# Kernel tuning notes

Hardware: AMD Instinct MI355X
Metric: run time of the kernel (lower is better)

The kernel has to match this reference:

```python
import jax, jax.numpy as jnp
import numpy as np
from jax import lax

ALPHA = 0.85
C1 = 0.01 ** 2
C2 = 0.03 ** 2


def _avg_pool3(x):
    # F.avg_pool2d(x, 3, 1, 1) with count_include_pad=True: zero-pad, divide by 9.
    s = lax.reduce_window(x, jnp.array(0.0, x.dtype), lax.add,
                          (1, 1, 3, 3), (1, 1, 1, 1),
                          [(0, 0), (0, 0), (1, 1), (1, 1)])
    return s / jnp.array(9.0, x.dtype)


def _ssim(x, y):
    mu_x = _avg_pool3(x)
    mu_y = _avg_pool3(y)
    sigma_x = jnp.clip(_avg_pool3(x * x) - mu_x * mu_x, 0.0, None)
    sigma_y = jnp.clip(_avg_pool3(y * y) - mu_y * mu_y, 0.0, None)
    sigma_xy = _avg_pool3(x * y) - mu_x * mu_y
    ssim_n = (2.0 * mu_x * mu_y + C1) * (2.0 * sigma_xy + C2)
    ssim_d = (mu_x * mu_x + mu_y * mu_y + C1) * (sigma_x + sigma_y + C2)
    return jnp.clip((1.0 - ssim_n / ssim_d) / 2.0, 0.0, 1.0)


def _warp_right(right_img, disp):
    # grid_sample(bilinear, border, align_corners=True) where y maps identically
    # to its own row -> a 1D horizontal bilinear gather at x_sample = x - disp.
    B, C, H, W = right_img.shape
    x_base = jnp.arange(W, dtype=disp.dtype).reshape(1, 1, 1, W)
    x_sample = x_base - disp                      # [B,1,H,W]
    xs = jnp.clip(x_sample, 0.0, W - 1.0)         # border padding
    x0 = jnp.floor(xs)
    w = xs - x0                                   # frac weight
    i0 = x0.astype(jnp.int32)
    i1 = jnp.minimum(i0 + 1, W - 1)
    i0b = jnp.broadcast_to(i0, (B, C, H, W))
    i1b = jnp.broadcast_to(i1, (B, C, H, W))
    g0 = jnp.take_along_axis(right_img, i0b, axis=3)
    g1 = jnp.take_along_axis(right_img, i1b, axis=3)
    warped = (1.0 - w) * g0 + w * g1              # w broadcasts over C
    valid = ((x_sample > 0) & (x_sample < W - 1)).astype(disp.dtype)
    return warped, valid


def setup_inputs() -> dict:
    key = jax.random.key(0)
    k1, k2, k3 = jax.random.split(key, 3)
    B, H, W = 8, 720, 1280
    disp = jax.random.normal(k1, (B, 1, H, W), dtype=jnp.float32)
    left_img = jax.random.uniform(k2, (B, 3, H, W), dtype=jnp.float32)
    right_img = jax.random.uniform(k3, (B, 3, H, W), dtype=jnp.float32)
    return {"disp": disp, "left_img": left_img, "right_img": right_img}


def reference(disp, left_img, right_img):
    right_warped, valid = _warp_right(right_img, disp)
    l1_err = jnp.mean(jnp.abs(left_img - right_warped), axis=1, keepdims=True)
    ssim_err = jnp.mean(_ssim(left_img, right_warped), axis=1, keepdims=True)
    photo_err = ALPHA * ssim_err + (1.0 - ALPHA) * l1_err
    n_valid = jnp.maximum(jnp.sum(valid), 1.0)
    return jnp.sum(photo_err * valid) / n_valid
```

## Files before the change

kernel.cpp:

```cpp
#include <hip/hip_runtime.h>


#define P_ALPHA 0.85f
#define P_C1 1e-4f
#define P_C2 9e-4f

constexpr int COLS  = 62;
constexpr int RPW   = 15;
constexpr int WAVES = 4;

__global__ __launch_bounds__(256, 6)
void photo_loss_kernel(const float* __restrict__ disp,
                       const float* __restrict__ left,
                       const float* __restrict__ right,
                       float* __restrict__ acc,
                       int H, int W)
{
    __shared__ float redpv[WAVES];
    __shared__ float redv[WAVES];

    const int tid  = threadIdx.x;
    const int lane = tid & 63;
    const int w    = tid >> 6;
    const int b    = blockIdx.z;
    const int col  = blockIdx.x * COLS + lane - 1;
    const int rowStart = (blockIdx.y * WAVES + w) * RPW;

    const int planeHW = H * W;
    const float* __restrict__ dispb = disp  + b * planeHW;
    const float* __restrict__ L0 = left  + (b * 3 + 0) * planeHW;
    const float* __restrict__ L1 = left  + (b * 3 + 1) * planeHW;
    const float* __restrict__ L2 = left  + (b * 3 + 2) * planeHW;
    const float* __restrict__ R0 = right + (b * 3 + 0) * planeHW;
    const float* __restrict__ R1 = right + (b * 3 + 1) * planeHW;
    const float* __restrict__ R2 = right + (b * 3 + 2) * planeHW;

    const float wm1f = (float)(W - 1);
    const int   colC = min(max(col, 0), W - 1);
    const float colv = (col >= 0 && col < W) ? 1.f : 0.f;
    const float ocm  = (lane >= 1 && lane <= COLS && col < W) ? 1.f : 0.f;

    float Ax0=0.f,Ay0=0.f,Axx0=0.f,Ayy0=0.f,Axy0=0.f;
    float Ax1=0.f,Ay1=0.f,Axx1=0.f,Ayy1=0.f,Axy1=0.f;
    float Ax2=0.f,Ay2=0.f,Axx2=0.f,Ayy2=0.f,Axy2=0.f;
    float Bx0=0.f,By0=0.f,Bxx0=0.f,Byy0=0.f,Bxy0=0.f;
    float Bx1=0.f,By1=0.f,Bxx1=0.f,Byy1=0.f,Bxy1=0.f;
    float Bx2=0.f,By2=0.f,Bxx2=0.f,Byy2=0.f,Bxy2=0.f;
    float l1P=0.f, vP=0.f;

    float sum_pv = 0.f, sum_v = 0.f;

    float gN0,gN1,gN2,gN3,gN4,gN5, frN, vmN, xN0,xN1,xN2;
    float dN;
    int   offN;

    {
        const int   rc0  = max(rowStart - 1, 0);
        const int   off0 = rc0 * W + colC;
        const float d0   = dispb[off0];
        xN0 = L0[off0]; xN1 = L1[off0]; xN2 = L2[off0];
        offN = rowStart * W + colC;
        dN   = dispb[offN];
        const float xs  = (float)col - d0;
        const float xcl = fminf(fmaxf(xs, 0.f), wm1f);
        const float xf  = floorf(xcl);
        frN = xcl - xf;
        const int i0 = (int)xf;
        const int i1 = min(i0 + 1, W - 1);
        const int ro = rc0 * W;
        gN0 = R0[ro + i0]; gN1 = R0[ro + i1];
        gN2 = R1[ro + i0]; gN3 = R1[ro + i1];
        gN4 = R2[ro + i0]; gN5 = R2[ro + i1];
        vmN = (xs > 0.f && xs < wm1f) ? 1.f : 0.f;
    }

    #pragma unroll 2
    for (int j = 0; j < RPW + 2; ++j) {
        const int r = rowStart - 1 + j;

        const float g0=gN0,g1=gN1,g2=gN2,g3=gN3,g4=gN4,g5=gN5;
        const float fr=frN, vm=vmN, xc0=xN0, xc1=xN1, xc2=xN2;

        if (j <= RPW) {
            const float xs  = (float)col - dN;
            const float xcl = fminf(fmaxf(xs, 0.f), wm1f);
            const float xf  = floorf(xcl);
            frN = xcl - xf;
            const int i0 = (int)xf;
            const int i1 = min(i0 + 1, W - 1);
            const int ro = offN - colC;
            gN0 = R0[ro + i0]; gN1 = R0[ro + i1];
            gN2 = R1[ro + i0]; gN3 = R1[ro + i1];
            gN4 = R2[ro + i0]; gN5 = R2[ro + i1];
            vmN = (xs > 0.f && xs < wm1f) ? 1.f : 0.f;
            xN0 = L0[offN]; xN1 = L1[offN]; xN2 = L2[offN];
            const int rc2 = min(r + 2, H - 1);
            offN = rc2 * W + colC;
            dN   = dispb[offN];
        }

        const float rv  = (r >= 0 && r < H) ? 1.f : 0.f;
        const float m   = rv * colv;
        const float omf = 1.f - fr;
        const float y0 = (omf * g0 + fr * g1) * m;
        const float y1 = (omf * g2 + fr * g3) * m;
        const float y2 = (omf * g4 + fr * g5) * m;
        const float x0 = xc0 * m;
        const float x1 = xc1 * m;
        const float x2 = xc2 * m;

        float Cx0,Cy0,Cxx0,Cyy0,Cxy0;
        float Cx1,Cy1,Cxx1,Cyy1,Cxy1;
        float Cx2,Cy2,Cxx2,Cyy2,Cxy2;
        {
            const float xl = __shfl_up(x0,1,64), xr = __shfl_down(x0,1,64);
            const float yl = __shfl_up(y0,1,64), yr = __shfl_down(y0,1,64);
            Cx0  = xl + x0 + xr;
            Cy0  = yl + y0 + yr;
            Cxx0 = xl*xl + x0*x0 + xr*xr;
            Cyy0 = yl*yl + y0*y0 + yr*yr;
            Cxy0 = xl*yl + x0*y0 + xr*yr;
        }
        {
            const float xl = __shfl_up(x1,1,64), xr = __shfl_down(x1,1,64);
            const float yl = __shfl_up(y1,1,64), yr = __shfl_down(y1,1,64);
            Cx1  = xl + x1 + xr;
            Cy1  = yl + y1 + yr;
            Cxx1 = xl*xl + x1*x1 + xr*xr;
            Cyy1 = yl*yl + y1*y1 + yr*yr;
            Cxy1 = xl*yl + x1*y1 + xr*yr;
        }
        {
            const float xl = __shfl_up(x2,1,64), xr = __shfl_down(x2,1,64);
            const float yl = __shfl_up(y2,1,64), yr = __shfl_down(y2,1,64);
            Cx2  = xl + x2 + xr;
            Cy2  = yl + y2 + yr;
            Cxx2 = xl*xl + x2*x2 + xr*xr;
            Cyy2 = yl*yl + y2*y2 + yr*yr;
            Cxy2 = xl*yl + x2*y2 + xr*yr;
        }
        const float l1C = fabsf(x0 - y0) + fabsf(x1 - y1) + fabsf(x2 - y2);
        const float vC  = vm;

        if (j >= 2) {
            const float inv9 = 1.f / 9.f;
            float ssim_sum = 0.f;
            #define SSIM_CH(SX,SY,SXX,SYY,SXY)                                   \
            {                                                                    \
                const float mu_x = (A##SX + B##SX + C##SX) * inv9;               \
                const float mu_y = (A##SY + B##SY + C##SY) * inv9;               \
                const float exx  = (A##SXX + B##SXX + C##SXX) * inv9;            \
                const float eyy  = (A##SYY + B##SYY + C##SYY) * inv9;            \
                const float exy  = (A##SXY + B##SXY + C##SXY) * inv9;            \
                const float sig_x  = fmaxf(exx - mu_x * mu_x, 0.f);              \
                const float sig_y  = fmaxf(eyy - mu_y * mu_y, 0.f);              \
                const float sig_xy = exy - mu_x * mu_y;                          \
                const float n  = (2.f*mu_x*mu_y + P_C1) * (2.f*sig_xy + P_C2);   \
                const float dd = (mu_x*mu_x + mu_y*mu_y + P_C1)                  \
                               * (sig_x + sig_y + P_C2);                         \
                float s = (1.f - n * __builtin_amdgcn_rcpf(dd)) * 0.5f;          \
                s = fminf(fmaxf(s, 0.f), 1.f);                                   \
                ssim_sum += s;                                                   \
            }
            SSIM_CH(x0,y0,xx0,yy0,xy0)
            SSIM_CH(x1,y1,xx1,yy1,xy1)
            SSIM_CH(x2,y2,xx2,yy2,xy2)
            #undef SSIM_CH
            const float photo = P_ALPHA * (ssim_sum * (1.f / 3.f))
                              + (1.f - P_ALPHA) * (l1P * (1.f / 3.f));
            sum_pv += photo * vP * ocm;
            sum_v  += vP * ocm;
        }

        Ax0=Bx0; Ay0=By0; Axx0=Bxx0; Ayy0=Byy0; Axy0=Bxy0;
        Ax1=Bx1; Ay1=By1; Axx1=Bxx1; Ayy1=Byy1; Axy1=Bxy1;
        Ax2=Bx2; Ay2=By2; Axx2=Bxx2; Ayy2=Byy2; Axy2=Bxy2;
        Bx0=Cx0; By0=Cy0; Bxx0=Cxx0; Byy0=Cyy0; Bxy0=Cxy0;
        Bx1=Cx1; By1=Cy1; Bxx1=Cxx1; Byy1=Cyy1; Bxy1=Cxy1;
        Bx2=Cx2; By2=Cy2; Bxx2=Cxx2; Byy2=Cyy2; Bxy2=Cxy2;
        l1P = l1C; vP = vC;
    }

    #pragma unroll
    for (int off = 32; off > 0; off >>= 1) {
        sum_pv += __shfl_down(sum_pv, off, 64);
        sum_v  += __shfl_down(sum_v,  off, 64);
    }
    if (lane == 0) { redpv[w] = sum_pv; redv[w] = sum_v; }
    __syncthreads();
    if (tid == 0) {
        atomicAdd(&acc[0], redpv[0] + redpv[1] + redpv[2] + redpv[3]);
        atomicAdd(&acc[1], redv[0]  + redv[1]  + redv[2]  + redv[3]);
    }
}

__global__ void photo_loss_finalize(const float* __restrict__ acc,
                                    float* __restrict__ out)
{
    out[0] = acc[0] / fmaxf(acc[1], 1.f);
}

extern "C" void kernel_launch(void* const* d_in, const int* in_sizes, int n_in,
                              void* d_out, int out_size, void* d_ws, size_t ws_size,
                              hipStream_t stream)
{
    const float* disp  = (const float*)d_in[0];
    const float* left  = (const float*)d_in[1];
    const float* right = (const float*)d_in[2];
    float* out = (float*)d_out;
    float* acc = (float*)d_ws;

    const int B = 8, H = 720, W = 1280;

    hipMemsetAsync(acc, 0, 2 * sizeof(float), stream);

    dim3 grid((W + COLS - 1) / COLS, H / (WAVES * RPW), B);
    dim3 block(256);
    photo_loss_kernel<<<grid, block, 0, stream>>>(disp, left, right, acc, H, W);
    photo_loss_finalize<<<1, 1, 0, stream>>>(acc, out);
}
```

Baseline: 260.8 us.

## Stage right-image row window in LDS for warp gathers with global fallback

Each wave now loads a padded 80-column window of the three right-image channels per row into double-buffered shared memory using coalesced loads, prefetching one row ahead. The bilinear gathers read from LDS, and lanes whose sample index falls outside the window fall back to direct global loads. This replaces scattered global gathers with coalesced loads plus LDS reads. In exchange it adds LDS traffic, extra registers and a divergent fallback path, and lowers the launch-bounds occupancy hint from 6 to 4.

```diff
diff --git a/kernel.cpp b/kernel.cpp
--- a/kernel.cpp
+++ b/kernel.cpp
@@ -8,14 +8,17 @@
 constexpr int COLS  = 62;
 constexpr int RPW   = 15;
 constexpr int WAVES = 4;
-
-__global__ __launch_bounds__(256, 6)
+constexpr int PADW  = 80;
+constexpr int NST   = 3 * PADW;
+
+__global__ __launch_bounds__(256, 4)
 void photo_loss_kernel(const float* __restrict__ disp,
                        const float* __restrict__ left,
                        const float* __restrict__ right,
                        float* __restrict__ acc,
                        int H, int W)
 {
+    __shared__ float stage[WAVES][2][NST];
     __shared__ float redpv[WAVES];
     __shared__ float redv[WAVES];
 
@@ -23,8 +26,10 @@
     const int lane = tid & 63;
     const int w    = tid >> 6;
     const int b    = blockIdx.z;
-    const int col  = blockIdx.x * COLS + lane - 1;
+    const int s0   = blockIdx.x * COLS;
+    const int col  = s0 + lane - 1;
     const int rowStart = (blockIdx.y * WAVES + w) * RPW;
+    const int W_LO = s0 - 9;
 
     const int planeHW = H * W;
     const float* __restrict__ dispb = disp  + b * planeHW;
@@ -36,9 +41,27 @@
     const float* __restrict__ R2 = right + (b * 3 + 2) * planeHW;
 
     const float wm1f = (float)(W - 1);
+    const float colf = (float)col;
     const int   colC = min(max(col, 0), W - 1);
     const float colv = (col >= 0 && col < W) ? 1.f : 0.f;
     const float ocm  = (lane >= 1 && lane <= COLS && col < W) ? 1.f : 0.f;
+
+    int  sOff[4];
+    int  sLds[4];
+    bool sAct[4];
+    #pragma unroll
+    for (int p = 0; p < 4; ++p) {
+        const int idx  = p * 64 + lane;
+        sAct[p] = (idx < NST);
+        const int idxc = min(idx, NST - 1);
+        const int ch   = idxc / PADW;
+        const int k    = idxc - ch * PADW;
+        const int srcCol = min(max(W_LO + k, 0), W - 1);
+        sOff[p] = (b * 3 + ch) * planeHW + srcCol;
+        sLds[p] = ch * PADW + k;
+    }
+    float* const buf0 = &stage[w][0][0];
+    float* const buf1 = &stage[w][1][0];
 
     float Ax0=0.f,Ay0=0.f,Axx0=0.f,Ayy0=0.f,Axy0=0.f;
     float Ax1=0.f,Ay1=0.f,Axx1=0.f,Ayy1=0.f,Axy1=0.f;
@@ -50,61 +73,72 @@
 
     float sum_pv = 0.f, sum_v = 0.f;
 
-    float gN0,gN1,gN2,gN3,gN4,gN5, frN, vmN, xN0,xN1,xN2;
-    float dN;
-    int   offN;
-
+    float sv0, sv1, sv2, sv3;
+    const int rc0 = max(rowStart - 1, 0);
     {
-        const int   rc0  = max(rowStart - 1, 0);
-        const int   off0 = rc0 * W + colC;
-        const float d0   = dispb[off0];
-        xN0 = L0[off0]; xN1 = L1[off0]; xN2 = L2[off0];
-        offN = rowStart * W + colC;
-        dN   = dispb[offN];
-        const float xs  = (float)col - d0;
-        const float xcl = fminf(fmaxf(xs, 0.f), wm1f);
-        const float xf  = floorf(xcl);
-        frN = xcl - xf;
-        const int i0 = (int)xf;
-        const int i1 = min(i0 + 1, W - 1);
         const int ro = rc0 * W;
-        gN0 = R0[ro + i0]; gN1 = R0[ro + i1];
-        gN2 = R1[ro + i0]; gN3 = R1[ro + i1];
-        gN4 = R2[ro + i0]; gN5 = R2[ro + i1];
-        vmN = (xs > 0.f && xs < wm1f) ? 1.f : 0.f;
+        sv0 = right[sOff[0] + ro];
+        sv1 = right[sOff[1] + ro];
+        sv2 = right[sOff[2] + ro];
+        sv3 = sAct[3] ? right[sOff[3] + ro] : 0.f;
+        buf0[sLds[0]] = sv0; buf0[sLds[1]] = sv1; buf0[sLds[2]] = sv2;
+        if (sAct[3]) buf0[sLds[3]] = sv3;
+    }
+    {
+        const int ro = rowStart * W;
+        sv0 = right[sOff[0] + ro];
+        sv1 = right[sOff[1] + ro];
+        sv2 = right[sOff[2] + ro];
+        if (sAct[3]) sv3 = right[sOff[3] + ro];
+    }
+    float dN, xN0, xN1, xN2;
+    {
+        const int off = rc0 * W + colC;
+        dN = dispb[off]; xN0 = L0[off]; xN1 = L1[off]; xN2 = L2[off];
     }
 
     #pragma unroll 2
     for (int j = 0; j < RPW + 2; ++j) {
         const int r = rowStart - 1 + j;
-
-        const float g0=gN0,g1=gN1,g2=gN2,g3=gN3,g4=gN4,g5=gN5;
-        const float fr=frN, vm=vmN, xc0=xN0, xc1=xN1, xc2=xN2;
+        float* const bufC = (j & 1) ? buf1 : buf0;
+        float* const bufN = (j & 1) ? buf0 : buf1;
+
+        const float d = dN, xc0 = xN0, xc1 = xN1, xc2 = xN2;
 
         if (j <= RPW) {
-            const float xs  = (float)col - dN;
-            const float xcl = fminf(fmaxf(xs, 0.f), wm1f);
-            const float xf  = floorf(xcl);
-            frN = xcl - xf;
-            const int i0 = (int)xf;
-            const int i1 = min(i0 + 1, W - 1);
-            const int ro = offN - colC;
-            gN0 = R0[ro + i0]; gN1 = R0[ro + i1];
-            gN2 = R1[ro + i0]; gN3 = R1[ro + i1];
-            gN4 = R2[ro + i0]; gN5 = R2[ro + i1];
-            vmN = (xs > 0.f && xs < wm1f) ? 1.f : 0.f;
-            xN0 = L0[offN]; xN1 = L1[offN]; xN2 = L2[offN];
-            const int rc2 = min(r + 2, H - 1);
-            offN = rc2 * W + colC;
-            dN   = dispb[offN];
+            const int rn  = min(r + 1, H - 1);
+            const int off = rn * W + colC;
+            dN = dispb[off]; xN0 = L0[off]; xN1 = L1[off]; xN2 = L2[off];
+        }
+
+        const float xs  = colf - d;
+        const float xcl = fminf(fmaxf(xs, 0.f), wm1f);
+        const float xf  = floorf(xcl);
+        const float fr  = xcl - xf;
+        const int   i0  = (int)xf;
+        const int   k   = i0 - W_LO;
+        const int   kc  = min(max(k, 0), PADW - 2);
+        float g00 = bufC[kc],            g01 = bufC[kc + 1];
+        float g10 = bufC[PADW + kc],     g11 = bufC[PADW + kc + 1];
+        float g20 = bufC[2 * PADW + kc], g21 = bufC[2 * PADW + kc + 1];
+        const bool bad = (k < 0) || (k > PADW - 2);
+        if (__builtin_expect(__any(bad), 0)) {
+            if (bad) {
+                const int rc = min(max(r, 0), H - 1);
+                const int ro = rc * W;
+                const int i1 = min(i0 + 1, W - 1);
+                g00 = R0[ro + i0]; g01 = R0[ro + i1];
+                g10 = R1[ro + i0]; g11 = R1[ro + i1];
+                g20 = R2[ro + i0]; g21 = R2[ro + i1];
+            }
         }
 
         const float rv  = (r >= 0 && r < H) ? 1.f : 0.f;
         const float m   = rv * colv;
         const float omf = 1.f - fr;
-        const float y0 = (omf * g0 + fr * g1) * m;
-        const float y1 = (omf * g2 + fr * g3) * m;
-        const float y2 = (omf * g4 + fr * g5) * m;
+        const float y0 = (omf * g00 + fr * g01) * m;
+        const float y1 = (omf * g10 + fr * g11) * m;
+        const float y2 = (omf * g20 + fr * g21) * m;
         const float x0 = xc0 * m;
         const float x1 = xc1 * m;
         const float x2 = xc2 * m;
@@ -140,7 +174,7 @@
             Cxy2 = xl*yl + x2*y2 + xr*yr;
         }
         const float l1C = fabsf(x0 - y0) + fabsf(x1 - y1) + fabsf(x2 - y2);
-        const float vC  = vm;
+        const float vC  = (xs > 0.f && xs < wm1f) ? 1.f : 0.f;
 
         if (j >= 2) {
             const float inv9 = 1.f / 9.f;
@@ -172,6 +206,19 @@
             sum_v  += vP * ocm;
         }
 
+        if (j <= RPW) {
+            bufN[sLds[0]] = sv0; bufN[sLds[1]] = sv1; bufN[sLds[2]] = sv2;
+            if (sAct[3]) bufN[sLds[3]] = sv3;
+        }
+        if (j <= RPW - 1) {
+            const int rs = min(r + 2, H - 1);
+            const int ro = rs * W;
+            sv0 = right[sOff[0] + ro];
+            sv1 = right[sOff[1] + ro];
+            sv2 = right[sOff[2] + ro];
+            if (sAct[3]) sv3 = right[sOff[3] + ro];
+        }
+
         Ax0=Bx0; Ay0=By0; Axx0=Bxx0; Ayy0=Byy0; Axy0=Bxy0;
         Ax1=Bx1; Ay1=By1; Axx1=Bxx1; Ayy1=Byy1; Axy1=Bxy1;
         Ax2=Bx2; Ay2=By2; Axx2=Bxx2; Ayy2=Byy2; Axy2=Bxy2;
```

Result: slower. 434.5 us (+66.6%).
